# Performance work log

Measured on AMD Instinct MI355X. Metric: run time of the kernel, lower is better.

The kernel has to match this reference:

```python
import jax, jax.numpy as jnp
import numpy as np

H = 1024  # hidden_dim; GRU hidden size is H+1, embedding_dim = 2*H


def _bigru_scan(h0, Wih_f, Whh_f, bih_f, bhh_f, Wih_b, Whh_b, bih_b, bhh_b):
    """h0: (T, 2, H+1). Runs the per-token recurrence of AnswerSynthesisEncoder.

    At each step the torch code feeds the previous step's output y (2H+2,) back
    in as the GRU *input* x = y[:2H].reshape(2,H).sum(0), and uses the token
    embedding (+f_s,f_e) reshaped to (2, H+1) as the initial hidden state h_0
    of the bidirectional, seq_len=1 GRU. Since h_0 does not depend on the
    carry, the hidden-side gate preactivations are precomputed as one GEMM.
    """
    Hh = H + 1
    gh_f = h0[:, 0] @ Whh_f.T + bhh_f  # (T, 3*(H+1))
    gh_b = h0[:, 1] @ Whh_b.T + bhh_b

    def cell(x, h, gh, Wih, bih):
        gi = Wih @ x + bih
        i_r, i_z, i_n = jnp.split(gi, 3)
        h_r, h_z, h_n = jnp.split(gh, 3)
        r = jax.nn.sigmoid(i_r + h_r)
        z = jax.nn.sigmoid(i_z + h_z)
        n = jnp.tanh(i_n + r * h_n)
        return (1.0 - z) * n + z * h

    def step(y, inp):
        h0_t, ghf_t, ghb_t = inp
        x = y[: 2 * H].reshape(2, H).sum(axis=0)  # (H,)
        yf = cell(x, h0_t[0], ghf_t, Wih_f, bih_f)
        yb = cell(x, h0_t[1], ghb_t, Wih_b, bih_b)
        y_new = jnp.concatenate([yf, yb])  # (2H+2,)
        return y_new, y_new

    y0 = jnp.zeros(2 * Hh, dtype=h0.dtype)
    _, outs = jax.lax.scan(step, y0, (h0, gh_f, gh_b))  # (T, 2H+2)
    # final slice: reshape(2, H+1)[:, :H] per token -> concat of both halves' first H
    return jnp.concatenate([outs[:, :H], outs[:, Hh : Hh + H]], axis=1)  # (T, 2H)


def setup_inputs() -> dict:
    key = jax.random.key(0)
    ks = jax.random.split(key, 12)
    Hh = H + 1
    s = 0.02
    return {
        "e_q": jax.random.normal(ks[0], (512, 2 * H), jnp.float32),
        "e_p": jax.random.normal(ks[1], (4096, 2 * H), jnp.float32),
        "f_s": jax.random.uniform(ks[2], (4096, 1), jnp.float32),
        "f_e": jax.random.uniform(ks[3], (4096, 1), jnp.float32),
        "Wih_f": jax.random.normal(ks[4], (3 * Hh, H), jnp.float32) * s,
        "Whh_f": jax.random.normal(ks[5], (3 * Hh, Hh), jnp.float32) * s,
        "bih_f": jax.random.normal(ks[6], (3 * Hh,), jnp.float32) * s,
        "bhh_f": jax.random.normal(ks[7], (3 * Hh,), jnp.float32) * s,
        "Wih_b": jax.random.normal(ks[8], (3 * Hh, H), jnp.float32) * s,
        "Whh_b": jax.random.normal(ks[9], (3 * Hh, Hh), jnp.float32) * s,
        "bih_b": jax.random.normal(ks[10], (3 * Hh,), jnp.float32) * s,
        "bhh_b": jax.random.normal(ks[11], (3 * Hh,), jnp.float32) * s,
    }


def reference(e_q, e_p, f_s, f_e, Wih_f, Whh_f, bih_f, bhh_f, Wih_b, Whh_b, bih_b, bhh_b):
    Hh = H + 1
    # h_0 per passage token: cat([e_p_t, f_s_t, f_e_t]).reshape(2, H+1)
    h0_p = jnp.concatenate([e_p, f_s, f_e], axis=1).reshape(-1, 2, Hh)
    # h_0 per query token: cat([e_q_t, 0, 0]).reshape(2, H+1)
    zq = jnp.zeros((e_q.shape[0], 2), e_q.dtype)
    h0_q = jnp.concatenate([e_q, zq], axis=1).reshape(-1, 2, Hh)
    h_p = _bigru_scan(h0_p, Wih_f, Whh_f, bih_f, bhh_f, Wih_b, Whh_b, bih_b, bhh_b)
    h_q = _bigru_scan(h0_q, Wih_f, Whh_f, bih_f, bhh_f, Wih_b, Whh_b, bih_b, bhh_b)
    return (h_q, h_p)
```

## Files before the change

### kernel.cpp

```cpp
#include <hip/hip_runtime.h>
#include <stdint.h>


#define H    1024
#define HH   1025
#define N3   3075
#define TQ   512
#define TP   4096
#define MTOT 4608
#define GTOT 2050
#define GH_ELEMS (MTOT * N3)
#define AKP  1056
#define ATOT ((size_t)MTOT * 2 * AKP)

typedef unsigned long long ull;
typedef __attribute__((ext_vector_type(8))) short short8;
typedef __attribute__((ext_vector_type(4))) float f32x4;

__device__ __forceinline__ float sigm(float x) { return 1.f / (1.f + __expf(-x)); }
__device__ __forceinline__ float fast_tanh(float x) {
    float e = __expf(2.f * x);
    return (e - 1.f) / (e + 1.f);
}
__device__ __forceinline__ unsigned short f2bf(float f) {
    unsigned u = __float_as_uint(f);
    unsigned r = (u + 0x7FFFu + ((u >> 16) & 1u)) >> 16;
    return (unsigned short)r;
}
__device__ __forceinline__ float bf2f(unsigned short h) {
    return __uint_as_float(((unsigned)h) << 16);
}

#define ALOAD(p)     __hip_atomic_load((p), __ATOMIC_RELAXED, __HIP_MEMORY_SCOPE_AGENT)
#define ASTORE(p, v) __hip_atomic_store((p), (v), __ATOMIC_RELAXED, __HIP_MEMORY_SCOPE_AGENT)

__global__ __launch_bounds__(256) void prep_abf(
    const float* __restrict__ eq, const float* __restrict__ ep,
    const float* __restrict__ fs, const float* __restrict__ fe,
    unsigned short* __restrict__ abf)
{
    const int K8 = AKP / 8;
    int idx = blockIdx.x * 256 + threadIdx.x;
    int rowid = idx / K8;
    if (rowid >= MTOT * 2) return;
    int k0 = (idx - rowid * K8) * 8;
    int dir = rowid & 1;
    int m = rowid >> 1;
    bool isq = m < TQ;
    const float* e = isq ? eq : ep;
    int t = isq ? m : m - TQ;

    short8 hi, lo;
#pragma unroll
    for (int j = 0; j < 8; j++) {
        int gk = k0 + j;
        float v = 0.f;
        if (gk < HH) {
            if (dir == 0)            v = e[(size_t)t * 2048 + gk];
            else if (gk < 1023)      v = e[(size_t)t * 2048 + 1025 + gk];
            else if (!isq)           v = (gk == 1023) ? fs[t] : fe[t];
        }
        unsigned short h = f2bf(v);
        hi[j] = (short)h;
        lo[j] = (short)f2bf(v - bf2f(h));
    }
    size_t base = (size_t)rowid * AKP + k0;
    *(short8*)&abf[base] = hi;
    *(short8*)&abf[ATOT + base] = lo;
}

__global__ __launch_bounds__(256, 2) void gh_gemm_fast(
    const unsigned short* __restrict__ abf,
    const float* __restrict__ Whh_f, const float* __restrict__ bhh_f,
    const float* __restrict__ Whh_b, const float* __restrict__ bhh_b,
    float* __restrict__ ghf, float* __restrict__ ghb)
{
    const int dir = blockIdx.z;
    const float* W  = dir ? Whh_b : Whh_f;
    const float* bh = dir ? bhh_b : bhh_f;
    float* gh = dir ? ghb : ghf;
    const int n0 = blockIdx.x * 128;
    const int m0 = blockIdx.y * 128;
    const int tid = threadIdx.x, wave = tid >> 6, lane = tid & 63;

    __shared__ __align__(16) unsigned short Ah[128][40];
    __shared__ __align__(16) unsigned short Al[128][40];
    __shared__ __align__(16) unsigned short Bs[128][40];

    f32x4 acc[2][8];
#pragma unroll
    for (int rt = 0; rt < 2; rt++)
#pragma unroll
        for (int c = 0; c < 8; c++) acc[rt][c] = (f32x4){0.f, 0.f, 0.f, 0.f};

    for (int kc = 0; kc < 33; kc++) {
        const int k0 = kc * 32;
        {
            int r = tid >> 1, h16 = (tid & 1) * 16;
            size_t arow = ((size_t)(m0 + r) * 2 + dir) * AKP + k0 + h16;
            short8 v0 = *(const short8*)&abf[arow];
            short8 v1 = *(const short8*)&abf[arow + 8];
            *(short8*)&Ah[r][h16]     = v0;
            *(short8*)&Ah[r][h16 + 8] = v1;
            short8 u0 = *(const short8*)&abf[ATOT + arow];
            short8 u1 = *(const short8*)&abf[ATOT + arow + 8];
            *(short8*)&Al[r][h16]     = u0;
            *(short8*)&Al[r][h16 + 8] = u1;
        }
#pragma unroll
        for (int u = 0; u < 16; u++) {
            int lin = u * 256 + tid;
            int r = lin >> 5, k = lin & 31;
            int gr = n0 + r, gk = k0 + k;
            float v = (gr < N3 && gk < HH) ? W[(size_t)gr * HH + gk] : 0.f;
            Bs[r][k] = f2bf(v);
        }
        __syncthreads();

        const int rA0 = wave * 32 + (lane & 15);
        const int ko  = (lane >> 4) * 8;
        short8 ah0 = *(const short8*)&Ah[rA0][ko];
        short8 ah1 = *(const short8*)&Ah[rA0 + 16][ko];
        short8 al0 = *(const short8*)&Al[rA0][ko];
        short8 al1 = *(const short8*)&Al[rA0 + 16][ko];
#pragma unroll
        for (int c = 0; c < 8; c++) {
            short8 b = *(const short8*)&Bs[c * 16 + (lane & 15)][ko];
            acc[0][c] = __builtin_amdgcn_mfma_f32_16x16x32_bf16(ah0, b, acc[0][c], 0, 0, 0);
            acc[0][c] = __builtin_amdgcn_mfma_f32_16x16x32_bf16(al0, b, acc[0][c], 0, 0, 0);
            acc[1][c] = __builtin_amdgcn_mfma_f32_16x16x32_bf16(ah1, b, acc[1][c], 0, 0, 0);
            acc[1][c] = __builtin_amdgcn_mfma_f32_16x16x32_bf16(al1, b, acc[1][c], 0, 0, 0);
        }
        __syncthreads();
    }

#pragma unroll
    for (int rt = 0; rt < 2; rt++)
#pragma unroll
    for (int c = 0; c < 8; c++) {
        int col = n0 + c * 16 + (lane & 15);
        if (col < N3) {
            float bias = bh[col];
#pragma unroll
            for (int j = 0; j < 4; j++) {
                int row = m0 + wave * 32 + rt * 16 + (lane >> 4) * 4 + j;
                gh[(size_t)row * N3 + col] = acc[rt][c][j] + bias;
            }
        }
    }
}

__global__ __launch_bounds__(256, 2) void gh_gemm_mfma(
    const float* __restrict__ eq, const float* __restrict__ ep,
    const float* __restrict__ fs, const float* __restrict__ fe,
    const float* __restrict__ Whh_f, const float* __restrict__ bhh_f,
    const float* __restrict__ Whh_b, const float* __restrict__ bhh_b,
    float* __restrict__ ghf, float* __restrict__ ghb)
{
    const int dir = blockIdx.z;
    const float* W  = dir ? Whh_b : Whh_f;
    const float* bh = dir ? bhh_b : bhh_f;
    float* gh = dir ? ghb : ghf;
    const int n0 = blockIdx.x * 128;
    const int m0 = blockIdx.y * 64;
    const int tid  = threadIdx.x;
    const int wave = tid >> 6;
    const int lane = tid & 63;

    __shared__ __align__(16) unsigned short Ah[64][40];
    __shared__ __align__(16) unsigned short Al[64][40];
    __shared__ __align__(16) unsigned short Bs[128][40];

    f32x4 acc[8];
#pragma unroll
    for (int c = 0; c < 8; c++) acc[c] = (f32x4){0.f, 0.f, 0.f, 0.f};

    for (int kc = 0; kc < 33; kc++) {
        const int k0 = kc * 32;
#pragma unroll
        for (int u = 0; u < 8; u++) {
            int lin = u * 256 + tid;
            int row = lin >> 5, k = lin & 31;
            int gm = m0 + row, gk = k0 + k;
            float v = 0.f;
            if (gk < HH) {
                bool isq = gm < TQ;
                const float* e = isq ? eq : ep;
                int t = isq ? gm : gm - TQ;
                if (dir == 0)            v = e[(size_t)t * 2048 + gk];
                else if (gk < 1023)      v = e[(size_t)t * 2048 + 1025 + gk];
                else if (!isq)           v = (gk == 1023) ? fs[t] : fe[t];
            }
            unsigned short h = f2bf(v);
            Ah[row][k] = h;
            Al[row][k] = f2bf(v - bf2f(h));
        }
#pragma unroll
        for (int u = 0; u < 16; u++) {
            int lin = u * 256 + tid;
            int r = lin >> 5, k = lin & 31;
            int gr = n0 + r, gk = k0 + k;
            float v = (gr < N3 && gk < HH) ? W[(size_t)gr * HH + gk] : 0.f;
            Bs[r][k] = f2bf(v);
        }
        __syncthreads();

        const int arow = wave * 16 + (lane & 15);
        const int koff = (lane >> 4) * 8;
        short8 ah = *(const short8*)&Ah[arow][koff];
        short8 al = *(const short8*)&Al[arow][koff];
#pragma unroll
        for (int c = 0; c < 8; c++) {
            short8 b = *(const short8*)&Bs[c * 16 + (lane & 15)][koff];
            acc[c] = __builtin_amdgcn_mfma_f32_16x16x32_bf16(ah, b, acc[c], 0, 0, 0);
            acc[c] = __builtin_amdgcn_mfma_f32_16x16x32_bf16(al, b, acc[c], 0, 0, 0);
        }
        __syncthreads();
    }

#pragma unroll
    for (int c = 0; c < 8; c++) {
        int col = n0 + c * 16 + (lane & 15);
        if (col < N3) {
            float bias = bh[col];
#pragma unroll
            for (int r = 0; r < 4; r++) {
                int row = m0 + wave * 16 + (lane >> 4) * 4 + r;
                gh[(size_t)row * N3 + col] = acc[c][r] + bias;
            }
        }
    }
}

__global__ __launch_bounds__(256, 1) void bigru_scan(
    const float* __restrict__ eq, const float* __restrict__ ep,
    const float* __restrict__ fs, const float* __restrict__ fe,
    const float* __restrict__ Wih_f, const float* __restrict__ bih_f,
    const float* __restrict__ Wih_b, const float* __restrict__ bih_b,
    const float* __restrict__ ghf, const float* __restrict__ ghb,
    ull* __restrict__ comm,
    float* __restrict__ out)
{
    __shared__ float xsh[2][2][1024];

    const int tid  = threadIdx.x;
    const int wave = tid >> 6;
    const int lane = tid & 63;
    const int gbase = blockIdx.x * 12 + wave * 3;

    float wreg[9][16];
    float breg[9];
    int   dre[3], je[3];
    bool  vale[3];
#pragma unroll
    for (int e = 0; e < 3; e++) {
        int g = gbase + e;
        bool v = (g < GTOT);
        int gc = v ? g : 0;
        int dir = gc / HH;
        int j = gc % HH;
        dre[e] = dir; je[e] = j; vale[e] = v;
        const float* Wih = dir ? Wih_b : Wih_f;
        const float* bih = dir ? bih_b : bih_f;
#pragma unroll
        for (int gate = 0; gate < 3; gate++) {
            const float* wr = Wih + (size_t)(gate * HH + j) * H;
#pragma unroll
            for (int i = 0; i < 4; i++) {
                float4 w4 = *(const float4*)(wr + i * 256 + lane * 4);
                wreg[e * 3 + gate][i * 4 + 0] = w4.x;
                wreg[e * 3 + gate][i * 4 + 1] = w4.y;
                wreg[e * 3 + gate][i * 4 + 2] = w4.z;
                wreg[e * 3 + gate][i * 4 + 3] = w4.w;
            }
            breg[e * 3 + gate] = bih[gate * HH + j];
        }
    }

    int sgh[3], sh0[3], sspec[3];
#pragma unroll
    for (int e = 0; e < 3; e++) {
        sgh[e]   = __builtin_amdgcn_readfirstlane(dre[e] * GH_ELEMS + je[e]);
        sh0[e]   = __builtin_amdgcn_readfirstlane(dre[e] ? (1025 + je[e]) : je[e]);
        sspec[e] = __builtin_amdgcn_readfirstlane(
                       (dre[e] && je[e] >= 1023) ? (je[e] - 1022) : 0);
    }
    const float* ghAll = ghf;

    float ghcP[9], h0cP[3], ghcQ[9], h0cQ[3];

    auto loadP = [&](int tt, float gh9[9], float h03[3]) {
        size_t base = (size_t)(TQ + tt) * N3;
#pragma unroll
        for (int e = 0; e < 3; e++) {
#pragma unroll
            for (int gate = 0; gate < 3; gate++)
                gh9[e * 3 + gate] = ghAll[base + (size_t)sgh[e] + gate * HH];
            h03[e] = (sspec[e] == 0) ? ep[(size_t)tt * 2048 + sh0[e]]
                   : (sspec[e] == 1) ? fs[tt] : fe[tt];
        }
    };
    auto loadQ = [&](int tt, float gh9[9], float h03[3]) {
        size_t base = (size_t)tt * N3;
#pragma unroll
        for (int e = 0; e < 3; e++) {
#pragma unroll
            for (int gate = 0; gate < 3; gate++)
                gh9[e * 3 + gate] = ghAll[base + (size_t)sgh[e] + gate * HH];
            h03[e] = (sspec[e] == 0) ? eq[(size_t)tt * 2048 + sh0[e]] : 0.f;
        }
    };

    loadP(0, ghcP, h0cP);
    loadQ(0, ghcQ, h0cQ);

    ull* commP = comm;
    ull* commQ = comm + 2 * GTOT;

    int idx[8];
#pragma unroll
    for (int u = 0; u < 4; u++) {
        int j = tid + 256 * u;
        idx[2 * u]     = j;
        idx[2 * u + 1] = (j == 0) ? 1024 : (1024 + j);
    }

    for (int t = 0; t < TP; t++) {
        const bool doq = (t < TQ);
        const int par = t & 1;
        const int slot = (t + 1) & 1;
        const unsigned tag = (unsigned)t;
        ull* cp = commP + slot * GTOT;
        ull* cq = commQ + slot * GTOT;

        if (t == 0) {
#pragma unroll
            for (int u = 0; u < 4; u++) {
                int j = tid + 256 * u;
                xsh[par][0][j] = 0.f;
                xsh[par][1][j] = 0.f;
            }
        } else {
            ull vp[8];
#pragma unroll
            for (int u = 0; u < 8; u++) vp[u] = ALOAD(&cp[idx[u]]);
            bool done = false;
            while (!done) {
                done = true;
#pragma unroll
                for (int u = 0; u < 8; u++) {
                    if ((unsigned)(vp[u] >> 32) != tag) {
                        done = false;
                        vp[u] = ALOAD(&cp[idx[u]]);
                    }
                }
            }
#pragma unroll
            for (int u = 0; u < 4; u++) {
                int j = tid + 256 * u;
                xsh[par][0][j] = __uint_as_float((unsigned)vp[2 * u]) +
                                 __uint_as_float((unsigned)vp[2 * u + 1]);
            }
        }
        __syncthreads();

        ull vq[8];
        if (doq && t > 0) {
#pragma unroll
            for (int u = 0; u < 8; u++) vq[u] = ALOAD(&cq[idx[u]]);
            __builtin_amdgcn_sched_barrier(0);
        }

        float ghnP[9], h0nP[3], ghnQ[9], h0nQ[3];
        const bool ldn = (t + 1) < TP;
        const bool ldq = (t + 1) < TQ;
        if (ldn) loadP(t + 1, ghnP, h0nP);
        if (ldq) loadQ(t + 1, ghnQ, h0nQ);

        float accp[9];
        {
            float x[16];
#pragma unroll
            for (int i = 0; i < 4; i++) {
                float4 x4 = *(const float4*)&xsh[par][0][i * 256 + lane * 4];
                x[i * 4 + 0] = x4.x; x[i * 4 + 1] = x4.y;
                x[i * 4 + 2] = x4.z; x[i * 4 + 3] = x4.w;
            }
#pragma unroll
            for (int r = 0; r < 9; r++) {
                float s = 0.f;
#pragma unroll
                for (int i = 0; i < 16; i++) s += wreg[r][i] * x[i];
                accp[r] = s;
            }
        }
#pragma unroll
        for (int r = 0; r < 9; r++) {
            float v = accp[r];
#pragma unroll
            for (int off = 32; off > 0; off >>= 1) v += __shfl_xor(v, off, 64);
            accp[r] = v + breg[r];
        }

        const ull tagout = ((ull)(unsigned)(t + 1)) << 32;
        float yP[3], yQ[3];
#pragma unroll
        for (int e = 0; e < 3; e++) {
            float r = sigm(accp[e * 3 + 0] + ghcP[e * 3 + 0]);
            float z = sigm(accp[e * 3 + 1] + ghcP[e * 3 + 1]);
            float n = fast_tanh(accp[e * 3 + 2] + r * ghcP[e * 3 + 2]);
            yP[e] = (1.f - z) * n + z * h0cP[e];
            if (lane == 0 && vale[e]) {
                ull pk = tagout | (ull)__float_as_uint(yP[e]);
                ASTORE(&commP[par * GTOT + (gbase + e)], pk);
            }
        }

        if (doq) {
            if (t > 0) {
                bool done = false;
                while (!done) {
                    done = true;
#pragma unroll
                    for (int u = 0; u < 8; u++) {
                        if ((unsigned)(vq[u] >> 32) != tag) {
                            done = false;
                            vq[u] = ALOAD(&cq[idx[u]]);
                        }
                    }
                }
#pragma unroll
                for (int u = 0; u < 4; u++) {
                    int j = tid + 256 * u;
                    xsh[par][1][j] = __uint_as_float((unsigned)vq[2 * u]) +
                                     __uint_as_float((unsigned)vq[2 * u + 1]);
                }
            }
            __syncthreads();

            float accq[9];
            {
                float x[16];
#pragma unroll
                for (int i = 0; i < 4; i++) {
                    float4 x4 = *(const float4*)&xsh[par][1][i * 256 + lane * 4];
                    x[i * 4 + 0] = x4.x; x[i * 4 + 1] = x4.y;
                    x[i * 4 + 2] = x4.z; x[i * 4 + 3] = x4.w;
                }
#pragma unroll
                for (int r = 0; r < 9; r++) {
                    float s = 0.f;
#pragma unroll
                    for (int i = 0; i < 16; i++) s += wreg[r][i] * x[i];
#pragma unroll
                    for (int off = 32; off > 0; off >>= 1) s += __shfl_xor(s, off, 64);
                    accq[r] = s + breg[r];
                }
            }
#pragma unroll
            for (int e = 0; e < 3; e++) {
                float r = sigm(accq[e * 3 + 0] + ghcQ[e * 3 + 0]);
                float z = sigm(accq[e * 3 + 1] + ghcQ[e * 3 + 1]);
                float n = fast_tanh(accq[e * 3 + 2] + r * ghcQ[e * 3 + 2]);
                yQ[e] = (1.f - z) * n + z * h0cQ[e];
                if (lane == 0 && vale[e]) {
                    ull pk = tagout | (ull)__float_as_uint(yQ[e]);
                    ASTORE(&commQ[par * GTOT + (gbase + e)], pk);
                }
            }
        }

        if (lane == 0) {
#pragma unroll
            for (int e = 0; e < 3; e++) {
                if (vale[e] && je[e] < H) {
                    out[(size_t)TQ * 2048 + (size_t)t * 2048 + dre[e] * H + je[e]] = yP[e];
                    if (doq)
                        out[(size_t)t * 2048 + dre[e] * H + je[e]] = yQ[e];
                }
            }
        }

        if (ldn) {
#pragma unroll
            for (int i = 0; i < 9; i++) ghcP[i] = ghnP[i];
#pragma unroll
            for (int e = 0; e < 3; e++) h0cP[e] = h0nP[e];
        }
        if (ldq) {
#pragma unroll
            for (int i = 0; i < 9; i++) ghcQ[i] = ghnQ[i];
#pragma unroll
            for (int e = 0; e < 3; e++) h0cQ[e] = h0nQ[e];
        }
    }
}

extern "C" void kernel_launch(void* const* d_in, const int* in_sizes, int n_in,
                              void* d_out, int out_size, void* d_ws, size_t ws_size,
                              hipStream_t stream) {
    const float* eq    = (const float*)d_in[0];
    const float* ep    = (const float*)d_in[1];
    const float* fs    = (const float*)d_in[2];
    const float* fe    = (const float*)d_in[3];
    const float* Wih_f = (const float*)d_in[4];
    const float* Whh_f = (const float*)d_in[5];
    const float* bih_f = (const float*)d_in[6];
    const float* bhh_f = (const float*)d_in[7];
    const float* Wih_b = (const float*)d_in[8];
    const float* Whh_b = (const float*)d_in[9];
    const float* bih_b = (const float*)d_in[10];
    const float* bhh_b = (const float*)d_in[11];
    float* out = (float*)d_out;

    float* ghf = (float*)d_ws;
    float* ghb = ghf + (size_t)GH_ELEMS;
    size_t commOff = ((2 * (size_t)GH_ELEMS * sizeof(float)) + 4095) & ~(size_t)4095;
    ull* comm = (ull*)((char*)d_ws + commOff);
    size_t abfOff = (commOff + (size_t)4 * GTOT * sizeof(ull) + 4095) & ~(size_t)4095;
    size_t abfBytes = 2 * ATOT * sizeof(unsigned short);
    unsigned short* abf = (unsigned short*)((char*)d_ws + abfOff);
    const bool fastOK = (ws_size >= abfOff + abfBytes);

    hipMemsetAsync(comm, 0, (size_t)4 * GTOT * sizeof(ull), stream);

    if (fastOK) {
        int prepBlocks = (MTOT * 2 * (AKP / 8) + 255) / 256;
        prep_abf<<<dim3(prepBlocks), 256, 0, stream>>>(eq, ep, fs, fe, abf);
        gh_gemm_fast<<<dim3((N3 + 127) / 128, MTOT / 128, 2), 256, 0, stream>>>(
            abf, Whh_f, bhh_f, Whh_b, bhh_b, ghf, ghb);
    } else {
        gh_gemm_mfma<<<dim3((N3 + 127) / 128, MTOT / 64, 2), 256, 0, stream>>>(
            eq, ep, fs, fe, Whh_f, bhh_f, Whh_b, bhh_b, ghf, ghb);
    }

    bigru_scan<<<dim3(171), dim3(256), 0, stream>>>(
        eq, ep, fs, fe, Wih_f, bih_f, Wih_b, bih_b, ghf, ghb, comm, out);
}
```

Baseline: 16.49 ms.

## Split query and passage recurrences into separate persistent block groups

```diff
diff --git a/kernel.cpp b/kernel.cpp
--- a/kernel.cpp
+++ b/kernel.cpp
@@ -241,12 +241,14 @@
     ull* __restrict__ comm,
     float* __restrict__ out)
 {
-    __shared__ float xsh[2][2][1024];
+    __shared__ float xsh[2][1024];
 
     const int tid  = threadIdx.x;
     const int wave = tid >> 6;
     const int lane = tid & 63;
-    const int gbase = blockIdx.x * 12 + wave * 3;
+    const bool isP = ((int)blockIdx.x < 171);
+    const int cb   = isP ? (int)blockIdx.x : ((int)blockIdx.x - 171);
+    const int gbase = cb * 12 + wave * 3;
 
     float wreg[9][16];
     float breg[9];
@@ -287,8 +289,6 @@
     }
     const float* ghAll = ghf;
 
-    float ghcP[9], h0cP[3], ghcQ[9], h0cQ[3];
-
     auto loadP = [&](int tt, float gh9[9], float h03[3]) {
         size_t base = (size_t)(TQ + tt) * N3;
 #pragma unroll
@@ -311,113 +311,134 @@
         }
     };
 
-    loadP(0, ghcP, h0cP);
-    loadQ(0, ghcQ, h0cQ);
-
     ull* commP = comm;
     ull* commQ = comm + 2 * GTOT;
 
-    int idx[8];
-#pragma unroll
-    for (int u = 0; u < 4; u++) {
-        int j = tid + 256 * u;
-        idx[2 * u]     = j;
-        idx[2 * u + 1] = (j == 0) ? 1024 : (1024 + j);
-    }
-
-    for (int t = 0; t < TP; t++) {
-        const bool doq = (t < TQ);
-        const int par = t & 1;
-        const int slot = (t + 1) & 1;
-        const unsigned tag = (unsigned)t;
-        ull* cp = commP + slot * GTOT;
-        ull* cq = commQ + slot * GTOT;
-
-        if (t == 0) {
-#pragma unroll
-            for (int u = 0; u < 4; u++) {
-                int j = tid + 256 * u;
-                xsh[par][0][j] = 0.f;
-                xsh[par][1][j] = 0.f;
-            }
-        } else {
-            ull vp[8];
-#pragma unroll
-            for (int u = 0; u < 8; u++) vp[u] = ALOAD(&cp[idx[u]]);
-            bool done = false;
-            while (!done) {
-                done = true;
-#pragma unroll
-                for (int u = 0; u < 8; u++) {
-                    if ((unsigned)(vp[u] >> 32) != tag) {
-                        done = false;
-                        vp[u] = ALOAD(&cp[idx[u]]);
+    if (isP) {
+        float ghc[9], h0c[3];
+        loadP(0, ghc, h0c);
+
+        for (int t = 0; t < TP; t++) {
+            const int par = t & 1;
+
+            if (t == 0) {
+#pragma unroll
+                for (int u = 0; u < 4; u++) xsh[par][tid + 256 * u] = 0.f;
+            } else {
+                const int slot = (t + 1) & 1;
+                const unsigned tag = (unsigned)t;
+                ull* cp = commP + slot * GTOT;
+                int idx[8];
+#pragma unroll
+                for (int u = 0; u < 4; u++) {
+                    int j = tid + 256 * u;
+                    idx[2 * u]     = j;
+                    idx[2 * u + 1] = (j == 0) ? 1024 : (1024 + j);
+                }
+                ull vp[8];
+#pragma unroll
+                for (int u = 0; u < 8; u++) vp[u] = ALOAD(&cp[idx[u]]);
+                bool done = false;
+                while (!done) {
+                    done = true;
+#pragma unroll
+                    for (int u = 0; u < 8; u++) {
+                        if ((unsigned)(vp[u] >> 32) != tag) {
+                            done = false;
+                            vp[u] = ALOAD(&cp[idx[u]]);
+                        }
                     }
                 }
-            }
-#pragma unroll
-            for (int u = 0; u < 4; u++) {
-                int j = tid + 256 * u;
-                xsh[par][0][j] = __uint_as_float((unsigned)vp[2 * u]) +
-                                 __uint_as_float((unsigned)vp[2 * u + 1]);
-            }
-        }
-        __syncthreads();
-
-        ull vq[8];
-        if (doq && t > 0) {
-#pragma unroll
-            for (int u = 0; u < 8; u++) vq[u] = ALOAD(&cq[idx[u]]);
-            __builtin_amdgcn_sched_barrier(0);
-        }
-
-        float ghnP[9], h0nP[3], ghnQ[9], h0nQ[3];
-        const bool ldn = (t + 1) < TP;
-        const bool ldq = (t + 1) < TQ;
-        if (ldn) loadP(t + 1, ghnP, h0nP);
-        if (ldq) loadQ(t + 1, ghnQ, h0nQ);
-
-        float accp[9];
-        {
-            float x[16];
-#pragma unroll
-            for (int i = 0; i < 4; i++) {
-                float4 x4 = *(const float4*)&xsh[par][0][i * 256 + lane * 4];
-                x[i * 4 + 0] = x4.x; x[i * 4 + 1] = x4.y;
-                x[i * 4 + 2] = x4.z; x[i * 4 + 3] = x4.w;
+#pragma unroll
+                for (int u = 0; u < 4; u++) {
+                    int j = tid + 256 * u;
+                    xsh[par][j] = __uint_as_float((unsigned)vp[2 * u]) +
+                                  __uint_as_float((unsigned)vp[2 * u + 1]);
+                }
+            }
+            __syncthreads();
+
+            float ghn[9], h0n[3];
+            const bool ldn = (t + 1) < TP;
+            if (ldn) loadP(t + 1, ghn, h0n);
+
+            float accp[9];
+            {
+                float x[16];
+#pragma unroll
+                for (int i = 0; i < 4; i++) {
+                    float4 x4 = *(const float4*)&xsh[par][i * 256 + lane * 4];
+                    x[i * 4 + 0] = x4.x; x[i * 4 + 1] = x4.y;
+                    x[i * 4 + 2] = x4.z; x[i * 4 + 3] = x4.w;
+                }
+#pragma unroll
+                for (int r = 0; r < 9; r++) {
+                    float s = 0.f;
+#pragma unroll
+                    for (int i = 0; i < 16; i++) s += wreg[r][i] * x[i];
+                    accp[r] = s;
+                }
             }
 #pragma unroll
             for (int r = 0; r < 9; r++) {
-                float s = 0.f;
-#pragma unroll
-                for (int i = 0; i < 16; i++) s += wreg[r][i] * x[i];
-                accp[r] = s;
-            }
-        }
-#pragma unroll
-        for (int r = 0; r < 9; r++) {
-            float v = accp[r];
-#pragma unroll
-            for (int off = 32; off > 0; off >>= 1) v += __shfl_xor(v, off, 64);
-            accp[r] = v + breg[r];
-        }
-
-        const ull tagout = ((ull)(unsigned)(t + 1)) << 32;
-        float yP[3], yQ[3];
-#pragma unroll
-        for (int e = 0; e < 3; e++) {
-            float r = sigm(accp[e * 3 + 0] + ghcP[e * 3 + 0]);
-            float z = sigm(accp[e * 3 + 1] + ghcP[e * 3 + 1]);
-            float n = fast_tanh(accp[e * 3 + 2] + r * ghcP[e * 3 + 2]);
-            yP[e] = (1.f - z) * n + z * h0cP[e];
-            if (lane == 0 && vale[e]) {
-                ull pk = tagout | (ull)__float_as_uint(yP[e]);
-                ASTORE(&commP[par * GTOT + (gbase + e)], pk);
-            }
-        }
-
-        if (doq) {
-            if (t > 0) {
+                float v = accp[r];
+#pragma unroll
+                for (int off = 32; off > 0; off >>= 1) v += __shfl_xor(v, off, 64);
+                accp[r] = v + breg[r];
+            }
+
+            const ull tagout = ((ull)(unsigned)(t + 1)) << 32;
+            float yP[3];
+#pragma unroll
+            for (int e = 0; e < 3; e++) {
+                float r = sigm(accp[e * 3 + 0] + ghc[e * 3 + 0]);
+                float z = sigm(accp[e * 3 + 1] + ghc[e * 3 + 1]);
+                float n = fast_tanh(accp[e * 3 + 2] + r * ghc[e * 3 + 2]);
+                yP[e] = (1.f - z) * n + z * h0c[e];
+                if (lane == 0 && vale[e]) {
+                    ull pk = tagout | (ull)__float_as_uint(yP[e]);
+                    ASTORE(&commP[par * GTOT + (gbase + e)], pk);
+                }
+            }
+            if (lane == 0) {
+#pragma unroll
+                for (int e = 0; e < 3; e++) {
+                    if (vale[e] && je[e] < H)
+                        out[(size_t)TQ * 2048 + (size_t)t * 2048 + dre[e] * H + je[e]] = yP[e];
+                }
+            }
+
+            if (ldn) {
+#pragma unroll
+                for (int i = 0; i < 9; i++) ghc[i] = ghn[i];
+#pragma unroll
+                for (int e = 0; e < 3; e++) h0c[e] = h0n[e];
+            }
+        }
+    } else {
+        float ghc[9], h0c[3];
+        loadQ(0, ghc, h0c);
+
+        for (int t = 0; t < TQ; t++) {
+            const int par = t & 1;
+
+            if (t == 0) {
+#pragma unroll
+                for (int u = 0; u < 4; u++) xsh[par][tid + 256 * u] = 0.f;
+            } else {
+                const int slot = (t + 1) & 1;
+                const unsigned tag = (unsigned)t;
+                ull* cq = commQ + slot * GTOT;
+                int idx[8];
+#pragma unroll
+                for (int u = 0; u < 4; u++) {
+                    int j = tid + 256 * u;
+                    idx[2 * u]     = j;
+                    idx[2 * u + 1] = (j == 0) ? 1024 : (1024 + j);
+                }
+                ull vq[8];
+#pragma unroll
+                for (int u = 0; u < 8; u++) vq[u] = ALOAD(&cq[idx[u]]);
                 bool done = false;
                 while (!done) {
                     done = true;
@@ -432,18 +453,22 @@
 #pragma unroll
                 for (int u = 0; u < 4; u++) {
                     int j = tid + 256 * u;
-                    xsh[par][1][j] = __uint_as_float((unsigned)vq[2 * u]) +
-                                     __uint_as_float((unsigned)vq[2 * u + 1]);
+                    xsh[par][j] = __uint_as_float((unsigned)vq[2 * u]) +
+                                  __uint_as_float((unsigned)vq[2 * u + 1]);
                 }
             }
             __syncthreads();
+
+            float ghn[9], h0n[3];
+            const bool ldn = (t + 1) < TQ;
+            if (ldn) loadQ(t + 1, ghn, h0n);
 
             float accq[9];
             {
                 float x[16];
 #pragma unroll
                 for (int i = 0; i < 4; i++) {
-                    float4 x4 = *(const float4*)&xsh[par][1][i * 256 + lane * 4];
+                    float4 x4 = *(const float4*)&xsh[par][i * 256 + lane * 4];
                     x[i * 4 + 0] = x4.x; x[i * 4 + 1] = x4.y;
                     x[i * 4 + 2] = x4.z; x[i * 4 + 3] = x4.w;
                 }
@@ -452,46 +477,44 @@
                     float s = 0.f;
 #pragma unroll
                     for (int i = 0; i < 16; i++) s += wreg[r][i] * x[i];
-#pragma unroll
-                    for (int off = 32; off > 0; off >>= 1) s += __shfl_xor(s, off, 64);
-                    accq[r] = s + breg[r];
-                }
-            }
+                    accq[r] = s;
+                }
+            }
+#pragma unroll
+            for (int r = 0; r < 9; r++) {
+                float v = accq[r];
+#pragma unroll
+                for (int off = 32; off > 0; off >>= 1) v += __shfl_xor(v, off, 64);
+                accq[r] = v + breg[r];
+            }
+
+            const ull tagout = ((ull)(unsigned)(t + 1)) << 32;
+            float yQ[3];
 #pragma unroll
             for (int e = 0; e < 3; e++) {
-                float r = sigm(accq[e * 3 + 0] + ghcQ[e * 3 + 0]);
-                float z = sigm(accq[e * 3 + 1] + ghcQ[e * 3 + 1]);
-                float n = fast_tanh(accq[e * 3 + 2] + r * ghcQ[e * 3 + 2]);
-                yQ[e] = (1.f - z) * n + z * h0cQ[e];
+                float r = sigm(accq[e * 3 + 0] + ghc[e * 3 + 0]);
+                float z = sigm(accq[e * 3 + 1] + ghc[e * 3 + 1]);
+                float n = fast_tanh(accq[e * 3 + 2] + r * ghc[e * 3 + 2]);
+                yQ[e] = (1.f - z) * n + z * h0c[e];
                 if (lane == 0 && vale[e]) {
                     ull pk = tagout | (ull)__float_as_uint(yQ[e]);
                     ASTORE(&commQ[par * GTOT + (gbase + e)], pk);
                 }
             }
-        }
-
-        if (lane == 0) {
-#pragma unroll
-            for (int e = 0; e < 3; e++) {
-                if (vale[e] && je[e] < H) {
-                    out[(size_t)TQ * 2048 + (size_t)t * 2048 + dre[e] * H + je[e]] = yP[e];
-                    if (doq)
+            if (lane == 0) {
+#pragma unroll
+                for (int e = 0; e < 3; e++) {
+                    if (vale[e] && je[e] < H)
                         out[(size_t)t * 2048 + dre[e] * H + je[e]] = yQ[e];
                 }
             }
-        }
-
-        if (ldn) {
-#pragma unroll
-            for (int i = 0; i < 9; i++) ghcP[i] = ghnP[i];
-#pragma unroll
-            for (int e = 0; e < 3; e++) h0cP[e] = h0nP[e];
-        }
-        if (ldq) {
-#pragma unroll
-            for (int i = 0; i < 9; i++) ghcQ[i] = ghnQ[i];
-#pragma unroll
-            for (int e = 0; e < 3; e++) h0cQ[e] = h0nQ[e];
+
+            if (ldn) {
+#pragma unroll
+                for (int i = 0; i < 9; i++) ghc[i] = ghn[i];
+#pragma unroll
+                for (int e = 0; e < 3; e++) h0c[e] = h0n[e];
+            }
         }
     }
 }
@@ -534,6 +557,6 @@
             eq, ep, fs, fe, Whh_f, bhh_f, Whh_b, bhh_b, ghf, ghb);
     }
 
-    bigru_scan<<<dim3(171), dim3(256), 0, stream>>>(
+    bigru_scan<<<dim3(342), dim3(256), 0, stream>>>(
         eq, ep, fs, fe, Wih_f, bih_f, Wih_b, bih_b, ghf, ghb, comm, out);
 }
```

Result: slower. 19.21 ms (+16.5%).
